# Kernel tuning notes

Measured on AMD Instinct MI355X. Metric: run time of the kernel, lower is better.

The kernel has to match this reference:

```python
import jax, jax.numpy as jnp
import numpy as np

ROBOT_W = 1.0
PHASE_W = 1.0
COHER_W = 10.0
SPEED_W = 5.0
MAX_SPEED = 10.0
SMOOTH_VEL_W = 0.05
SMOOTH_ACC_W = 0.01

# illegal phase transitions {(0,2),(1,0),(2,0),(2,1)} as a 3x3 lookup table
_ILLEGAL = np.zeros((3, 3), dtype=bool)
for a, b in [(0, 2), (1, 0), (2, 0), (2, 1)]:
    _ILLEGAL[a, b] = True
ILLEGAL_TABLE = jnp.asarray(_ILLEGAL)


def setup_inputs() -> dict:
    key = jax.random.key(0)
    k1, k2, k3, k4 = jax.random.split(key, 4)
    B, T = 256, 8192
    # scale by 8 so per-frame speeds (norm of diffs of 3-vectors) exceed MAX_SPEED
    pred_robot = jax.random.normal(k1, (B, T, 12), dtype=jnp.float32) * 8.0
    gt_robot = jax.random.normal(k2, (B, T, 12), dtype=jnp.float32) * 8.0
    pred_phase = jax.random.normal(k3, (B, T, 3), dtype=jnp.float32)
    gt_phase = jax.random.randint(k4, (B, T), 0, 3, dtype=jnp.int32)
    return {"pred_robot": pred_robot, "pred_phase": pred_phase,
            "gt_robot": gt_robot, "gt_phase": gt_phase}


def _coherence_loss(phase_logits):
    # vectorized replacement for the O(B*T) Python double loop
    p = jnp.argmax(phase_logits, axis=-1)            # [B, T]
    pt, pt1 = p[:, :-1], p[:, 1:]                    # [B, T-1]
    illegal = ILLEGAL_TABLE[pt, pt1]                 # [B, T-1] bool
    # logit of the (illegal) predicted phase at t+1
    sel = jnp.take_along_axis(phase_logits[:, 1:], pt1[..., None], axis=-1)[..., 0]
    loss_sum = jnp.sum(jnp.where(illegal, sel * sel, 0.0))
    count = jnp.sum(illegal)
    return jnp.where(count > 0, loss_sum / jnp.maximum(count, 1).astype(sel.dtype), 0.0)


def _speed_loss(pred_robot):
    B, T, D = pred_robot.shape
    vel = pred_robot[:, 1:] - pred_robot[:, :-1]     # [B, T-1, 12]
    pts = vel.reshape(B, T - 1, 4, 3)
    speeds = jnp.linalg.norm(pts, axis=-1)           # [B, T-1, 4]
    pen = jax.nn.relu(speeds - MAX_SPEED)
    return SPEED_W * jnp.mean(pen * pen)


def reference(pred_robot, pred_phase, gt_robot, gt_phase):
    # MSE over robot trajectory
    robot_loss = jnp.mean((pred_robot - gt_robot) ** 2)
    # cross-entropy over 3 phase classes
    logp = jax.nn.log_softmax(pred_phase, axis=-1)   # [B, T, 3]
    nll = -jnp.take_along_axis(logp, gt_phase[..., None].astype(jnp.int32), axis=-1)[..., 0]
    phase_loss = jnp.mean(nll)
    coherence = _coherence_loss(pred_phase)
    speed_loss = _speed_loss(pred_robot)
    vel = pred_robot[:, 1:] - pred_robot[:, :-1]
    vel_loss = jnp.mean(vel * vel)
    acc = pred_robot[:, 2:] - 2.0 * pred_robot[:, 1:-1] + pred_robot[:, :-2]
    acc_loss = jnp.mean(acc * acc)
    total = (ROBOT_W * robot_loss + PHASE_W * phase_loss + COHER_W * coherence
             + speed_loss + SMOOTH_VEL_W * vel_loss + SMOOTH_ACC_W * acc_loss)
    return total
```

## Files before the change

kernel.cpp:

```cpp
#include <hip/hip_runtime.h>
#include <math.h>

#define B_DIM 256
#define T_DIM 8192
#define BLOCK 256
#define NSLOT 256
#define GRID_BLOCKS 8192


__global__ __launch_bounds__(BLOCK) void combined_loss_main(
    const float4* __restrict__ pred4,
    const float*  __restrict__ pred_phase,
    const float4* __restrict__ gt4,
    const int*    __restrict__ gt_phase,
    double* __restrict__ ws)
{
    __shared__ float s_red[4][8];

    const int tid = threadIdx.x;
    const int r   = (int)blockIdx.x * BLOCK + tid;
    const int t   = r & (T_DIM - 1);
    const bool v1 = (t < T_DIM - 1);
    const bool v2 = (t < T_DIM - 2);

    const float4* pr = pred4 + (size_t)r * 3;
    const float4* gr = gt4   + (size_t)r * 3;
    const float*  pp = pred_phase + (size_t)r * 3;

    const int o1 = v1 ? 3 : 0;
    const int o2 = v2 ? 6 : 0;

    float4 a0 = pr[0],      a1 = pr[1],      a2 = pr[2];
    float4 b0 = pr[o1],     b1 = pr[o1 + 1], b2 = pr[o1 + 2];
    float4 c0 = pr[o2],     c1 = pr[o2 + 1], c2 = pr[o2 + 2];
    float4 q0 = gr[0],      q1 = gr[1],      q2 = gr[2];

    const float l0 = pp[0],  l1 = pp[1],  l2 = pp[2];
    const float n0 = pp[o1], n1 = pp[o1 + 1], n2 = pp[o1 + 2];
    const int gidx = gt_phase[r];

    float sse = 0.0f;
    {
        float d;
        d = a0.x - q0.x; sse += d*d;  d = a0.y - q0.y; sse += d*d;
        d = a0.z - q0.z; sse += d*d;  d = a0.w - q0.w; sse += d*d;
        d = a1.x - q1.x; sse += d*d;  d = a1.y - q1.y; sse += d*d;
        d = a1.z - q1.z; sse += d*d;  d = a1.w - q1.w; sse += d*d;
        d = a2.x - q2.x; sse += d*d;  d = a2.y - q2.y; sse += d*d;
        d = a2.z - q2.z; sse += d*d;  d = a2.w - q2.w; sse += d*d;
    }

    float m = fmaxf(l0, fmaxf(l1, l2));
    float lse = m + logf(expf(l0 - m) + expf(l1 - m) + expf(l2 - m));
    float sel = (gidx == 0) ? l0 : ((gidx == 1) ? l1 : l2);
    float nll = lse - sel;

    float csum = 0.0f, ccnt = 0.0f;
    if (v1) {
        int p = 0; float pm = l0;
        if (l1 > pm) { pm = l1; p = 1; }
        if (l2 > pm) { pm = l2; p = 2; }
        int p1 = 0; float m1 = n0;
        if (n1 > m1) { m1 = n1; p1 = 1; }
        if (n2 > m1) { m1 = n2; p1 = 2; }
        int mask = (p == 0) ? 4 : ((p == 1) ? 1 : 3);
        if ((mask >> p1) & 1) { csum = m1 * m1; ccnt = 1.0f; }
    }

    float pen2 = 0.0f, velsq = 0.0f, accsq = 0.0f;
    {
        float rA[12] = { a0.x,a0.y,a0.z,a0.w, a1.x,a1.y,a1.z,a1.w, a2.x,a2.y,a2.z,a2.w };
        float rB[12] = { b0.x,b0.y,b0.z,b0.w, b1.x,b1.y,b1.z,b1.w, b2.x,b2.y,b2.z,b2.w };
        float rC[12] = { c0.x,c0.y,c0.z,c0.w, c1.x,c1.y,c1.z,c1.w, c2.x,c2.y,c2.z,c2.w };

        if (v1) {
            float vel[12];
            #pragma unroll
            for (int k = 0; k < 12; ++k) { vel[k] = rB[k] - rA[k]; velsq += vel[k]*vel[k]; }

            #pragma unroll
            for (int j = 0; j < 4; ++j) {
                float sx = vel[3*j], sy = vel[3*j+1], sz = vel[3*j+2];
                float sp = sqrtf(sx*sx + sy*sy + sz*sz);
                float d = sp - 10.0f;
                if (d > 0.0f) pen2 += d*d;
            }

            if (v2) {
                #pragma unroll
                for (int k = 0; k < 12; ++k) {
                    float a = rC[k] - 2.0f*rB[k] + rA[k];
                    accsq += a*a;
                }
            }
        }
    }

    float vals[7] = { sse, nll, csum, ccnt, pen2, velsq, accsq };
    #pragma unroll
    for (int off = 32; off > 0; off >>= 1) {
        #pragma unroll
        for (int q = 0; q < 7; ++q)
            vals[q] += __shfl_down(vals[q], off, 64);
    }
    const int wave = tid >> 6, lane = tid & 63;
    if (lane == 0) {
        #pragma unroll
        for (int q = 0; q < 7; ++q) s_red[wave][q] = vals[q];
    }
    __syncthreads();
    if (tid < 7) {
        double acc = (double)s_red[0][tid] + (double)s_red[1][tid]
                   + (double)s_red[2][tid] + (double)s_red[3][tid];
        atomicAdd(&ws[(size_t)(blockIdx.x & (NSLOT - 1)) * 8 + tid], acc);
    }
}

__global__ __launch_bounds__(256) void combined_loss_final(
    const double* __restrict__ ws, float* __restrict__ out)
{
    __shared__ double sred[4][7];
    const int tid = threadIdx.x;
    double v[7];
    #pragma unroll
    for (int q = 0; q < 7; ++q) v[q] = ws[(size_t)tid * 8 + q];
    #pragma unroll
    for (int off = 32; off > 0; off >>= 1) {
        #pragma unroll
        for (int q = 0; q < 7; ++q)
            v[q] += __shfl_down(v[q], off, 64);
    }
    const int wave = tid >> 6, lane = tid & 63;
    if (lane == 0) {
        #pragma unroll
        for (int q = 0; q < 7; ++q) sred[wave][q] = v[q];
    }
    __syncthreads();
    if (tid == 0) {
        double s[7];
        #pragma unroll
        for (int q = 0; q < 7; ++q)
            s[q] = sred[0][q] + sred[1][q] + sred[2][q] + sred[3][q];
        const double robot = s[0] / (double)((size_t)B_DIM * T_DIM * 12);
        const double phase = s[1] / (double)((size_t)B_DIM * T_DIM);
        const double coher = (s[3] > 0.0) ? (s[2] / fmax(s[3], 1.0)) : 0.0;
        const double speed = 5.0  * (s[4] / (double)((size_t)B_DIM * (T_DIM - 1) * 4));
        const double vel   = 0.05 * (s[5] / (double)((size_t)B_DIM * (T_DIM - 1) * 12));
        const double acc   = 0.01 * (s[6] / (double)((size_t)B_DIM * (T_DIM - 2) * 12));
        out[0] = (float)(robot + phase + 10.0 * coher + speed + vel + acc);
    }
}

extern "C" void kernel_launch(void* const* d_in, const int* in_sizes, int n_in,
                              void* d_out, int out_size, void* d_ws, size_t ws_size,
                              hipStream_t stream)
{
    const float4* pred4      = (const float4*)d_in[0];
    const float*  pred_phase = (const float*)d_in[1];
    const float4* gt4        = (const float4*)d_in[2];
    const int*    gt_phase   = (const int*)d_in[3];
    double* ws  = (double*)d_ws;
    float*  out = (float*)d_out;

    hipMemsetAsync(d_ws, 0, (size_t)NSLOT * 8 * sizeof(double), stream);

    combined_loss_main<<<dim3(GRID_BLOCKS), BLOCK, 0, stream>>>(pred4, pred_phase, gt4, gt_phase, ws);
    combined_loss_final<<<1, 256, 0, stream>>>(ws, out);
}
```

Before: 237.7 us.

## Split robot and phase work into separate blocks with float4-per-thread coalesced loads

Replaces the one-thread-per-timestep mapping, where each thread loaded 12-float rows at a 48-byte stride, with a mapping where each thread handles one float4 of the flattened robot array. The thread reads neighbouring float4s to form velocity, acceleration and speed terms, and handles the 3-vector point straddling float4 boundaries through index arithmetic mod 3. Phase logits are handled by a separate set of blocks that read float4s and decode the 3-class rows. Each thread does 4 iterations. The goal is fully coalesced, vectorised loads and less redundant re-reading of neighbouring rows, at the cost of more index arithmetic and some branch divergence.

```diff
diff --git a/kernel.cpp b/kernel.cpp
--- a/kernel.cpp
+++ b/kernel.cpp
@@ -4,8 +4,15 @@
 #define B_DIM 256
 #define T_DIM 8192
 #define BLOCK 256
+#define ITERS 4
+#define RB_BLOCKS 6144
+#define PH_BLOCKS 1536
+#define GRID_BLOCKS (RB_BLOCKS + PH_BLOCKS)
 #define NSLOT 256
-#define GRID_BLOCKS 8192
+#define N4_ROBOT (B_DIM * T_DIM * 3)
+#define N4_PHASE (B_DIM * T_DIM * 3 / 4)
+#define BF4_ROBOT (T_DIM * 3)
+#define BF4_PHASE (T_DIM * 3 / 4)
 
 
 __global__ __launch_bounds__(BLOCK) void combined_loss_main(
@@ -16,82 +23,125 @@
     double* __restrict__ ws)
 {
     __shared__ float s_red[4][8];
-
     const int tid = threadIdx.x;
-    const int r   = (int)blockIdx.x * BLOCK + tid;
-    const int t   = r & (T_DIM - 1);
-    const bool v1 = (t < T_DIM - 1);
-    const bool v2 = (t < T_DIM - 2);
-
-    const float4* pr = pred4 + (size_t)r * 3;
-    const float4* gr = gt4   + (size_t)r * 3;
-    const float*  pp = pred_phase + (size_t)r * 3;
-
-    const int o1 = v1 ? 3 : 0;
-    const int o2 = v2 ? 6 : 0;
-
-    float4 a0 = pr[0],      a1 = pr[1],      a2 = pr[2];
-    float4 b0 = pr[o1],     b1 = pr[o1 + 1], b2 = pr[o1 + 2];
-    float4 c0 = pr[o2],     c1 = pr[o2 + 1], c2 = pr[o2 + 2];
-    float4 q0 = gr[0],      q1 = gr[1],      q2 = gr[2];
-
-    const float l0 = pp[0],  l1 = pp[1],  l2 = pp[2];
-    const float n0 = pp[o1], n1 = pp[o1 + 1], n2 = pp[o1 + 2];
-    const int gidx = gt_phase[r];
-
-    float sse = 0.0f;
-    {
-        float d;
-        d = a0.x - q0.x; sse += d*d;  d = a0.y - q0.y; sse += d*d;
-        d = a0.z - q0.z; sse += d*d;  d = a0.w - q0.w; sse += d*d;
-        d = a1.x - q1.x; sse += d*d;  d = a1.y - q1.y; sse += d*d;
-        d = a1.z - q1.z; sse += d*d;  d = a1.w - q1.w; sse += d*d;
-        d = a2.x - q2.x; sse += d*d;  d = a2.y - q2.y; sse += d*d;
-        d = a2.z - q2.z; sse += d*d;  d = a2.w - q2.w; sse += d*d;
-    }
-
-    float m = fmaxf(l0, fmaxf(l1, l2));
-    float lse = m + logf(expf(l0 - m) + expf(l1 - m) + expf(l2 - m));
-    float sel = (gidx == 0) ? l0 : ((gidx == 1) ? l1 : l2);
-    float nll = lse - sel;
-
-    float csum = 0.0f, ccnt = 0.0f;
-    if (v1) {
-        int p = 0; float pm = l0;
-        if (l1 > pm) { pm = l1; p = 1; }
-        if (l2 > pm) { pm = l2; p = 2; }
-        int p1 = 0; float m1 = n0;
-        if (n1 > m1) { m1 = n1; p1 = 1; }
-        if (n2 > m1) { m1 = n2; p1 = 2; }
-        int mask = (p == 0) ? 4 : ((p == 1) ? 1 : 3);
-        if ((mask >> p1) & 1) { csum = m1 * m1; ccnt = 1.0f; }
-    }
-
-    float pen2 = 0.0f, velsq = 0.0f, accsq = 0.0f;
-    {
-        float rA[12] = { a0.x,a0.y,a0.z,a0.w, a1.x,a1.y,a1.z,a1.w, a2.x,a2.y,a2.z,a2.w };
-        float rB[12] = { b0.x,b0.y,b0.z,b0.w, b1.x,b1.y,b1.z,b1.w, b2.x,b2.y,b2.z,b2.w };
-        float rC[12] = { c0.x,c0.y,c0.z,c0.w, c1.x,c1.y,c1.z,c1.w, c2.x,c2.y,c2.z,c2.w };
-
-        if (v1) {
-            float vel[12];
-            #pragma unroll
-            for (int k = 0; k < 12; ++k) { vel[k] = rB[k] - rA[k]; velsq += vel[k]*vel[k]; }
-
-            #pragma unroll
-            for (int j = 0; j < 4; ++j) {
-                float sx = vel[3*j], sy = vel[3*j+1], sz = vel[3*j+2];
-                float sp = sqrtf(sx*sx + sy*sy + sz*sz);
-                float d = sp - 10.0f;
-                if (d > 0.0f) pen2 += d*d;
-            }
-
-            if (v2) {
-                #pragma unroll
-                for (int k = 0; k < 12; ++k) {
-                    float a = rC[k] - 2.0f*rB[k] + rA[k];
-                    accsq += a*a;
+    const int bx  = (int)blockIdx.x;
+
+    float sse=0.f, nll=0.f, csum=0.f, ccnt=0.f, pen2=0.f, velsq=0.f, accsq=0.f;
+
+    if (bx < RB_BLOCKS) {
+        const int Jbase = bx * (BLOCK * ITERS);
+        const int jbase = (bx % 24) * (BLOCK * ITERS);
+        #pragma unroll
+        for (int it = 0; it < ITERS; ++it) {
+            const int o = it * BLOCK + tid;
+            const int J = Jbase + o;
+            const int j = jbase + o;
+
+            float4 p0 = pred4[J];
+            float4 g  = gt4[J];
+            float4 p1 = pred4[min(J + 1, N4_ROBOT - 1)];
+            float4 p3 = pred4[min(J + 3, N4_ROBOT - 1)];
+            float4 p4 = pred4[min(J + 4, N4_ROBOT - 1)];
+            float4 p6 = pred4[min(J + 6, N4_ROBOT - 1)];
+
+            float d;
+            d = p0.x - g.x; sse += d*d;  d = p0.y - g.y; sse += d*d;
+            d = p0.z - g.z; sse += d*d;  d = p0.w - g.w; sse += d*d;
+
+            const bool vv = j < (BF4_ROBOT - 3);
+            const bool va = j < (BF4_ROBOT - 6);
+
+            const float vx = p3.x - p0.x, vy = p3.y - p0.y;
+            const float vz = p3.z - p0.z, vw = p3.w - p0.w;
+            if (vv) velsq += vx*vx + vy*vy + vz*vz + vw*vw;
+
+            if (va) {
+                const float ax = p6.x - 2.f*p3.x + p0.x;
+                const float ay = p6.y - 2.f*p3.y + p0.y;
+                const float az = p6.z - 2.f*p3.z + p0.z;
+                const float aw = p6.w - 2.f*p3.w + p0.w;
+                accsq += ax*ax + ay*ay + az*az + aw*aw;
+            }
+
+            const float wx = p4.x - p1.x, wy = p4.y - p1.y;
+            const int s3 = j % 3;
+            const float c0x = (s3 == 0) ? vx : ((s3 == 1) ? vz : vy);
+            const float c0y = (s3 == 0) ? vy : ((s3 == 1) ? vw : vz);
+            const float c0z = (s3 == 0) ? vz : ((s3 == 1) ? wx : vw);
+            if (vv) {
+                const float sp0 = sqrtf(c0x*c0x + c0y*c0y + c0z*c0z);
+                const float d0 = sp0 - 10.f;
+                if (d0 > 0.f) pen2 += d0*d0;
+                if (s3 == 0) {
+                    const float sp1 = sqrtf(vw*vw + wx*wx + wy*wy);
+                    const float d1 = sp1 - 10.f;
+                    if (d1 > 0.f) pen2 += d1*d1;
                 }
+            }
+        }
+    } else {
+        const int pb    = bx - RB_BLOCKS;
+        const int batch = pb / 6;
+        const int Mbase = pb * (BLOCK * ITERS);
+        const int mbase = (pb % 6) * (BLOCK * ITERS);
+        const int bT    = batch * T_DIM;
+        const float4* ph4 = (const float4*)pred_phase;
+        #pragma unroll
+        for (int it = 0; it < ITERS; ++it) {
+            const int o = it * BLOCK + tid;
+            const int M = Mbase + o;
+            const int m = mbase + o;
+
+            float4 v  = ph4[M];
+            float4 nv = ph4[min(M + 1, N4_PHASE - 1)];
+            float4 nn = ph4[min(M + 2, N4_PHASE - 1)];
+
+            const int q = m / 3;
+            const int s = m - 3 * q;
+
+            const int   rA  = 4*q + ((s == 0) ? 0 : ((s == 1) ? 2 : 3));
+            const float la0 = (s == 0) ? v.x  : ((s == 1) ? v.z  : v.y);
+            const float la1 = (s == 0) ? v.y  : ((s == 1) ? v.w  : v.z);
+            const float la2 = (s == 0) ? v.z  : ((s == 1) ? nv.x : v.w);
+            const float na0 = (s == 0) ? v.w  : ((s == 1) ? nv.y : nv.x);
+            const float na1 = (s == 0) ? nv.x : ((s == 1) ? nv.z : nv.y);
+            const float na2 = (s == 0) ? nv.y : ((s == 1) ? nv.w : nv.z);
+
+            const int gA = gt_phase[bT + rA];
+            {
+                const float mx  = fmaxf(la0, fmaxf(la1, la2));
+                const float lse = mx + logf(expf(la0-mx) + expf(la1-mx) + expf(la2-mx));
+                const float sl  = (gA == 0) ? la0 : ((gA == 1) ? la1 : la2);
+                nll += lse - sl;
+            }
+            if (rA < T_DIM - 1) {
+                int p = 0; float pm = la0;
+                if (la1 > pm) { pm = la1; p = 1; }
+                if (la2 > pm) { pm = la2; p = 2; }
+                int p1 = 0; float m1 = na0;
+                if (na1 > m1) { m1 = na1; p1 = 1; }
+                if (na2 > m1) { m1 = na2; p1 = 2; }
+                const int mask = (p == 0) ? 4 : ((p == 1) ? 1 : 3);
+                if ((mask >> p1) & 1) { csum += m1*m1; ccnt += 1.f; }
+            }
+
+            if (s == 0) {
+                const int   rB  = 4*q + 1;
+                const float lb0 = v.w,  lb1 = nv.x, lb2 = nv.y;
+                const float nb0 = nv.z, nb1 = nv.w, nb2 = nn.x;
+                const int gB = gt_phase[bT + rB];
+                const float mx  = fmaxf(lb0, fmaxf(lb1, lb2));
+                const float lse = mx + logf(expf(lb0-mx) + expf(lb1-mx) + expf(lb2-mx));
+                const float sl  = (gB == 0) ? lb0 : ((gB == 1) ? lb1 : lb2);
+                nll += lse - sl;
+                int p = 0; float pm = lb0;
+                if (lb1 > pm) { pm = lb1; p = 1; }
+                if (lb2 > pm) { pm = lb2; p = 2; }
+                int p1 = 0; float m1 = nb0;
+                if (nb1 > m1) { m1 = nb1; p1 = 1; }
+                if (nb2 > m1) { m1 = nb2; p1 = 2; }
+                const int mask = (p == 0) ? 4 : ((p == 1) ? 1 : 3);
+                if ((mask >> p1) & 1) { csum += m1*m1; ccnt += 1.f; }
             }
         }
     }
@@ -112,7 +162,7 @@
     if (tid < 7) {
         double acc = (double)s_red[0][tid] + (double)s_red[1][tid]
                    + (double)s_red[2][tid] + (double)s_red[3][tid];
-        atomicAdd(&ws[(size_t)(blockIdx.x & (NSLOT - 1)) * 8 + tid], acc);
+        atomicAdd(&ws[(size_t)(bx & (NSLOT - 1)) * 8 + tid], acc);
     }
 }
 
```

Result: no change. 241.1 us (+1.4%).
